# Optimization experiments

Measured on AMD Instinct MI355X. Metric: run time of the kernel, lower is better.

Reference implementation:

```python
import jax, jax.numpy as jnp
import numpy as np

V, H, B, S = 32000, 512, 64, 128


def _cell(x, h, c, wih, whh, bih, bhh):
    # PyTorch LSTMCell: gates = x@Wih^T + bih + h@Whh^T + bhh; order i,f,g,o
    g = x @ wih.T + bih + h @ whh.T + bhh
    i, f, gg, o = jnp.split(g, 4, axis=-1)
    c2 = jax.nn.sigmoid(f) * c + jax.nn.sigmoid(i) * jnp.tanh(gg)
    return jax.nn.sigmoid(o) * jnp.tanh(c2), c2


def setup_inputs() -> dict:
    key = jax.random.key(0)
    ks = jax.random.split(key, 30)
    def nrm(k, shape, s=0.05):
        return jax.random.normal(k, shape, jnp.float32) * s
    a1 = float(np.sqrt(6.0 / (B + H)))      # xavier bound for [B, H] state
    a2 = float(np.sqrt(6.0 / (B + 2 * H)))  # xavier bound for [B, 2H] state
    return {
        "x": jax.random.randint(ks[0], (B, S), 0, V),
        "emb": nrm(ks[1], (V, H)),
        "h0f": jax.random.uniform(ks[2], (B, H), jnp.float32, -a1, a1),
        "c0f": jax.random.uniform(ks[3], (B, H), jnp.float32, -a1, a1),
        "h0b": jax.random.uniform(ks[4], (B, H), jnp.float32, -a1, a1),
        "c0b": jax.random.uniform(ks[5], (B, H), jnp.float32, -a1, a1),
        "h01": jax.random.uniform(ks[6], (B, 2 * H), jnp.float32, -a2, a2),
        "h02": jax.random.uniform(ks[7], (B, 2 * H), jnp.float32, -a2, a2),
        "c02": jax.random.uniform(ks[8], (B, 2 * H), jnp.float32, -a2, a2),
        "wih_f": nrm(ks[9], (4 * H, H)), "whh_f": nrm(ks[10], (4 * H, H)),
        "bih_f": nrm(ks[11], (4 * H,)), "bhh_f": nrm(ks[12], (4 * H,)),
        "wih_b": nrm(ks[13], (4 * H, H)), "whh_b": nrm(ks[14], (4 * H, H)),
        "bih_b": nrm(ks[15], (4 * H,)), "bhh_b": nrm(ks[16], (4 * H,)),
        "wih1": nrm(ks[17], (8 * H, 2 * H)), "whh1": nrm(ks[18], (8 * H, 2 * H)),
        "bih1": nrm(ks[19], (8 * H,)), "bhh1": nrm(ks[20], (8 * H,)),
        "wih2": nrm(ks[21], (8 * H, 2 * H)), "whh2": nrm(ks[22], (8 * H, 2 * H)),
        "bih2": nrm(ks[23], (8 * H,)), "bhh2": nrm(ks[24], (8 * H,)),
        "wlin": nrm(ks[25], (V, 2 * H)), "blin": nrm(ks[26], (V,)),
    }


def reference(x, emb, h0f, c0f, h0b, c0b, h01, h02, c02,
              wih_f, whh_f, bih_f, bhh_f, wih_b, whh_b, bih_b, bhh_b,
              wih1, whh1, bih1, bhh1, wih2, whh2, bih2, bhh2, wlin, blin):
    E = emb.at[0].set(0.0)           # padding_idx=0
    out = E[x].reshape(S, B, H)      # faithful to torch .view(seq, batch, -1)

    def fstep(carry, xt):
        h, c = _cell(xt, carry[0], carry[1], wih_f, whh_f, bih_f, bhh_f)
        return (h, c), h
    _, fwd = jax.lax.scan(fstep, (h0f, c0f), out)

    def bstep(carry, xt):
        h, c = _cell(xt, carry[0], carry[1], wih_b, whh_b, bih_b, bhh_b)
        return (h, c), h
    _, bwd = jax.lax.scan(bstep, (h0b, c0b), out[::-1])  # appended in reversed order

    def sstep(carry, fb):
        h1, h2, c2 = carry
        xin = jnp.concatenate([fb[0], fb[1]], axis=1)
        # faithful to source: lstm_1 is fed cs_lstm_2 as its cell state; its own c is discarded
        h1n, _c1 = _cell(xin, h1, c2, wih1, whh1, bih1, bhh1)
        # dropout(p=0.2) is identity in eval / reference mode
        h2n, c2n = _cell(h1n, h2, c2, wih2, whh2, bih2, bhh2)
        return (h1n, h2n, c2n), None
    (h1, h2, c2), _ = jax.lax.scan(sstep, (h01, h02, c02), (fwd, bwd))

    return h2 @ wlin.T + blin  # [B, V]
```

## Files before the change

### kernel.cpp

```cpp
#include <hip/hip_runtime.h>
#include <stdint.h>
#include <stddef.h>

typedef uint16_t u16_t;
typedef uint32_t u32_t;
typedef short s16x8 __attribute__((ext_vector_type(8)));
typedef uint16_t u16x4v __attribute__((ext_vector_type(4)));
typedef uint16_t u16x8v __attribute__((ext_vector_type(8)));
typedef float f32x4 __attribute__((ext_vector_type(4)));

#define DEV static __device__ __forceinline__

DEV u16_t f2bf(float f) {
  u32_t u = __float_as_uint(f);
  u += 0x7fffu + ((u >> 16) & 1u);
  return (u16_t)(u >> 16);
}
DEV float sig_(float x) { return 1.f / (1.f + __expf(-x)); }
DEV float th_(float x) {
  x = fminf(15.f, fmaxf(-15.f, x));
  float e = __expf(2.f * x);
  return (e - 1.f) / (e + 1.f);
}


__global__ void k_buildWC(const float* __restrict__ wih, const float* __restrict__ whh,
                          const float* __restrict__ bih, const float* __restrict__ bhh,
                          u16_t* __restrict__ WC, float* __restrict__ bs, int HH)
{
  const int K = HH * 2;
  const int nk8 = K >> 3;
  const long total = (long)HH * 4 * nk8;
  long idx = (long)blockIdx.x * blockDim.x + threadIdx.x;
  if (idx >= total) return;
  int p = (int)(idx / nk8);
  int k = (int)(idx - (long)p * nk8) << 3;
  int q = (p >> 4) & 3;
  int orig = q * HH + ((p >> 6) << 4) + (p & 15);
  const float* s = (k < HH) ? (wih + (size_t)orig * HH + k)
                            : (whh + (size_t)orig * HH + (k - HH));
  f32x4 a = *(const f32x4*)s;
  f32x4 b = *(const f32x4*)(s + 4);
  u16x8v o;
  o[0]=f2bf(a[0]); o[1]=f2bf(a[1]); o[2]=f2bf(a[2]); o[3]=f2bf(a[3]);
  o[4]=f2bf(b[0]); o[5]=f2bf(b[1]); o[6]=f2bf(b[2]); o[7]=f2bf(b[3]);
  *(u16x8v*)(WC + (size_t)p * K + k) = o;
  if (k == 0) bs[p] = bih[orig] + bhh[orig];
}

__global__ void k_init(const float* __restrict__ h0f, const float* __restrict__ h0b,
                       const float* __restrict__ h01, const float* __restrict__ h02,
                       u16_t* __restrict__ XIN0, u16_t* __restrict__ H1i, u16_t* __restrict__ H2i)
{
  int i = blockIdx.x * 256 + threadIdx.x;
  if (i >= 64 * 1024) return;
  int b = i >> 10, d = i & 1023;
  XIN0[i] = f2bf(d < 512 ? h0f[b * 512 + d] : h0b[b * 512 + (d - 512)]);
  H1i[i] = f2bf(h01[i]);
  H2i[i] = f2bf(h02[i]);
}

__global__ void k_emb(const int* __restrict__ x, const float* __restrict__ emb,
                      u16_t* __restrict__ Xemb)
{
  int idx = blockIdx.x * 256 + threadIdx.x;
  if (idx >= 524288) return;
  int sb = idx >> 6;
  int h0 = (idx & 63) << 3;
  int token = x[(sb >> 7) * 128 + (sb & 127)];
  u16x8v o = {0,0,0,0,0,0,0,0};
  if (token != 0) {
    const float* e = emb + (size_t)token * 512 + h0;
    f32x4 a = *(const f32x4*)e;
    f32x4 b = *(const f32x4*)(e + 4);
    o[0]=f2bf(a[0]); o[1]=f2bf(a[1]); o[2]=f2bf(a[2]); o[3]=f2bf(a[3]);
    o[4]=f2bf(b[0]); o[5]=f2bf(b[1]); o[6]=f2bf(b[2]); o[7]=f2bf(b[3]);
  }
  *(u16x8v*)(Xemb + (size_t)sb * 512 + h0) = o;
}

template<int W>
DEV void stage_chunkT(u16_t* smem, const u16_t* src, int ld, int wave, int lane)
{
#pragma unroll
  for (int j = 0; j < 64 / W; ++j) {
    int r = j * W + wave;
    s16x8 v = *(const s16x8*)(src + (size_t)r * ld + lane * 8);
    *(s16x8*)((char*)smem + r * 1024 + ((lane * 16) ^ ((r & 7) << 4))) = v;
  }
}

DEV s16x8 ld_afrag(const u16_t* smem, int m, int s, int lane)
{
  int r = m * 16 + (lane & 15);
  int off = (s * 64 + ((lane >> 4) << 4)) ^ ((r & 7) << 4);
  return *(const s16x8*)((const char*)smem + r * 1024 + off);
}

DEV void chunk_stream(u16_t* smem, f32x4 acc[4], const u16_t* a, int ld,
                      const u16_t* wptr, int wave, int lane)
{
  __syncthreads();
  stage_chunkT<8>(smem, a, ld, wave, lane);
  __syncthreads();
#pragma unroll
  for (int s = 0; s < 16; ++s) {
    s16x8 bf = *(const s16x8*)(wptr + s * 32);
#pragma unroll
    for (int m = 0; m < 4; ++m) {
      s16x8 af = ld_afrag(smem, m, s, lane);
      acc[m] = __builtin_amdgcn_mfma_f32_16x16x32_bf16(af, bf, acc[m], 0, 0, 0);
    }
  }
}

DEV void chunk_reg(u16_t* smem, f32x4 acc[4], const u16_t* a, int ld,
                   const s16x8 wr[16], int wave, int lane)
{
  __syncthreads();
  stage_chunkT<8>(smem, a, ld, wave, lane);
  __syncthreads();
#pragma unroll
  for (int s = 0; s < 16; ++s) {
#pragma unroll
    for (int m = 0; m < 4; ++m) {
      s16x8 af = ld_afrag(smem, m, s, lane);
      acc[m] = __builtin_amdgcn_mfma_f32_16x16x32_bf16(af, wr[s], acc[m], 0, 0, 0);
    }
  }
}

DEV void acc_to_ex(float* ex, const f32x4 acc[4], int wave, int lane)
{
#pragma unroll
  for (int m = 0; m < 4; ++m)
#pragma unroll
    for (int r = 0; r < 4; ++r)
      ex[wave * 1024 + (m * 16 + ((lane >> 4) << 2) + r) * 16 + (lane & 15)] = acc[m][r];
}

DEV void ast8(void* p, const void* v)
{
  unsigned long long u; __builtin_memcpy(&u, v, 8);
  __hip_atomic_store((unsigned long long*)p, u, __ATOMIC_RELAXED, __HIP_MEMORY_SCOPE_AGENT);
}

DEV void wait_flags(u32_t* f, int n, int tid)
{
  if (tid < 64) {
    int guard = 0;
    for (;;) {
      u32_t v = (tid < n) ? __hip_atomic_load(f + tid, __ATOMIC_RELAXED, __HIP_MEMORY_SCOPE_AGENT) : 1u;
      if (__all(v != 0)) break;
      if (++guard > (1 << 22)) break;
      __builtin_amdgcn_s_sleep(1);
    }
  }
  __builtin_amdgcn_fence(__ATOMIC_ACQUIRE, "workgroup");
  __syncthreads();
}

DEV void set_flag(u32_t* f, int tid)
{
  __syncthreads();
  if (tid == 0) {
    __builtin_amdgcn_fence(__ATOMIC_RELEASE, "workgroup");
    __hip_atomic_store(f, 1u, __ATOMIC_RELAXED, __HIP_MEMORY_SCOPE_AGENT);
  }
}

struct RP {
  const u16_t *WCf, *WCb, *WC1, *WC2;
  const float *bsf, *bsb, *bs1, *bs2;
  const u16_t *Xemb;
  u16_t *XIN, *H1, *H2;
  float *C2;
  u32_t *FLC, *FLA, *FLB;
  const float *c0f, *c0b, *c02;
};

__global__ __launch_bounds__(512, 2) void k_rnn(RP P)
{
  __shared__ u16_t smem[32768];
  const int tid = threadIdx.x;
  const int wave = tid >> 6, lane = tid & 63;
  const int wg = blockIdx.x;
  const int b  = tid >> 3;
  const int d0 = (tid & 7) << 2;
  const int gl = d0 >> 4;
  const int jj = d0 & 15;
  const f32x4 vzero = {0.f, 0.f, 0.f, 0.f};

  if (wg < 32) {
    const bool cfwd = wg < 16;
    const int G = cfwd ? wg : wg - 16;
    const u16_t* WCc = cfwd ? P.WCf : P.WCb;
    const float* bsc = cfwd ? P.bsf : P.bsb;
    const float* c0 = cfwd ? P.c0f : P.c0b;
    float c_cell[4];
#pragma unroll
    for (int i = 0; i < 4; ++i) c_cell[i] = c0[b * 512 + G * 32 + d0 + i];
    const u16_t* wrow = WCc + (size_t)(G * 128 + wave * 16 + (lane & 15)) * 1024
                        + ((lane >> 4) << 3);
    s16x8 wL[16];
#pragma unroll
    for (int s = 0; s < 16; ++s) wL[s] = *(const s16x8*)(wrow + 512 + s * 32);

    for (int t = 0; t < 128; ++t) {
      f32x4 acc[4] = {vzero, vzero, vzero, vzero};
      int trow = cfwd ? t : 127 - t;
      chunk_stream(smem, acc, P.Xemb + (size_t)trow * 32768, 512, wrow, wave, lane);
      if (t > 0) wait_flags(P.FLC + (t - 1) * 32 + (cfwd ? 0 : 16), 16, tid);
      chunk_reg(smem, acc, P.XIN + (size_t)t * 65536 + (cfwd ? 0 : 512), 1024, wL, wave, lane);
      __syncthreads();
      float* ex = (float*)smem;
      acc_to_ex(ex, acc, wave, lane);
      __syncthreads();
      u16x4v hv;
#pragma unroll
      for (int i = 0; i < 4; ++i) {
        int j = jj + i;
        float gq[4];
#pragma unroll
        for (int q = 0; q < 4; ++q)
          gq[q] = ex[(gl * 4 + q) * 1024 + b * 16 + j] + bsc[G * 128 + gl * 64 + q * 16 + j];
        float c = sig_(gq[1]) * c_cell[i] + sig_(gq[0]) * th_(gq[2]);
        c_cell[i] = c;
        hv[i] = f2bf(sig_(gq[3]) * th_(c));
      }
      ast8(P.XIN + (size_t)(t + 1) * 65536 + b * 1024 + (cfwd ? 0 : 512) + G * 32 + d0, &hv);
      set_flag(P.FLC + t * 32 + wg, tid);
    }
  } else if (wg < 64) {
    const int G = wg - 32;
    const u16_t* wrow = P.WC1 + (size_t)(G * 128 + wave * 16 + (lane & 15)) * 2048
                        + ((lane >> 4) << 3);
    s16x8 wL[32];
#pragma unroll
    for (int s = 0; s < 32; ++s) wL[s] = *(const s16x8*)(wrow + 1024 + s * 32);

    for (int u = 0; u < 128; ++u) {
      f32x4 acc[4] = {vzero, vzero, vzero, vzero};
      const u16_t* xin = P.XIN + (size_t)(u + 1) * 65536;
      wait_flags(P.FLC + u * 32, 16, tid);
      chunk_stream(smem, acc, xin, 1024, wrow, wave, lane);
      wait_flags(P.FLC + u * 32 + 16, 16, tid);
      chunk_stream(smem, acc, xin + 512, 1024, wrow + 512, wave, lane);
      if (u > 0) wait_flags(P.FLB + (u - 1) * 32 + G, 1, tid);
      const u16_t* h1p = P.H1 + (size_t)u * 65536;
      chunk_reg(smem, acc, h1p, 1024, wL, wave, lane);
      chunk_reg(smem, acc, h1p + 512, 1024, wL + 16, wave, lane);
      __syncthreads();
      float* ex = (float*)smem;
      acc_to_ex(ex, acc, wave, lane);
      __syncthreads();
      const float* c2p = (u == 0) ? (P.c02 + b * 1024 + G * 32 + d0)
                                  : (P.C2 + (size_t)u * 65536 + b * 1024 + G * 32 + d0);
      u16x4v hv;
#pragma unroll
      for (int i = 0; i < 4; ++i) {
        int j = jj + i;
        float gq[4];
#pragma unroll
        for (int q = 0; q < 4; ++q)
          gq[q] = ex[(gl * 4 + q) * 1024 + b * 16 + j] + P.bs1[G * 128 + gl * 64 + q * 16 + j];
        float c1 = sig_(gq[1]) * c2p[i] + sig_(gq[0]) * th_(gq[2]);
        hv[i] = f2bf(sig_(gq[3]) * th_(c1));
      }
      ast8(P.H1 + (size_t)(u + 1) * 65536 + b * 1024 + G * 32 + d0, &hv);
      set_flag(P.FLA + u * 32 + G, tid);
    }
  } else {
    const int G = wg - 64;
    const u16_t* wrow = P.WC2 + (size_t)(G * 128 + wave * 16 + (lane & 15)) * 2048
                        + ((lane >> 4) << 3);
    s16x8 wL[32];
#pragma unroll
    for (int s = 0; s < 32; ++s) wL[s] = *(const s16x8*)(wrow + s * 32);
    float c2r[4];
#pragma unroll
    for (int i = 0; i < 4; ++i) c2r[i] = P.c02[b * 1024 + G * 32 + d0 + i];

    for (int u = 0; u < 128; ++u) {
      f32x4 acc[4] = {vzero, vzero, vzero, vzero};
      const u16_t* h2p = P.H2 + (size_t)u * 65536;
      if (u > 0) wait_flags(P.FLB + (u - 1) * 32, 16, tid);
      chunk_stream(smem, acc, h2p, 1024, wrow + 1024, wave, lane);
      if (u > 0) wait_flags(P.FLB + (u - 1) * 32 + 16, 16, tid);
      chunk_stream(smem, acc, h2p + 512, 1024, wrow + 1536, wave, lane);
      const u16_t* h1n = P.H1 + (size_t)(u + 1) * 65536;
      wait_flags(P.FLA + u * 32, 16, tid);
      chunk_reg(smem, acc, h1n, 1024, wL, wave, lane);
      wait_flags(P.FLA + u * 32 + 16, 16, tid);
      chunk_reg(smem, acc, h1n + 512, 1024, wL + 16, wave, lane);
      __syncthreads();
      float* ex = (float*)smem;
      acc_to_ex(ex, acc, wave, lane);
      __syncthreads();
      u16x4v hv; float c2o[4];
#pragma unroll
      for (int i = 0; i < 4; ++i) {
        int j = jj + i;
        float gq[4];
#pragma unroll
        for (int q = 0; q < 4; ++q)
          gq[q] = ex[(gl * 4 + q) * 1024 + b * 16 + j] + P.bs2[G * 128 + gl * 64 + q * 16 + j];
        float c2n = sig_(gq[1]) * c2r[i] + sig_(gq[0]) * th_(gq[2]);
        c2r[i] = c2n; c2o[i] = c2n;
        hv[i] = f2bf(sig_(gq[3]) * th_(c2n));
      }
      ast8(P.H2 + (size_t)(u + 1) * 65536 + b * 1024 + G * 32 + d0, &hv);
      float* c2dst = P.C2 + (size_t)(u + 1) * 65536 + b * 1024 + G * 32 + d0;
      ast8(c2dst, &c2o[0]);
      ast8(c2dst + 2, &c2o[2]);
      set_flag(P.FLB + u * 32 + G, tid);
    }
  }
}

__global__ __launch_bounds__(256, 1) void k_logits(const u16_t* __restrict__ h2,
                                                   const float* __restrict__ wlin,
                                                   const float* __restrict__ blin,
                                                   float* __restrict__ out)
{
  __shared__ u16_t smem[32768];
  const int tid = threadIdx.x, wave = tid >> 6, lane = tid & 63;
  const int n0 = blockIdx.x * 128 + wave * 32;
  const f32x4 vzero = {0.f, 0.f, 0.f, 0.f};
  f32x4 acc[2][4];
#pragma unroll
  for (int nt = 0; nt < 2; ++nt)
#pragma unroll
    for (int m = 0; m < 4; ++m) acc[nt][m] = vzero;

  for (int c = 0; c < 2; ++c) {
    __syncthreads();
    stage_chunkT<4>(smem, h2 + c * 512, 1024, wave, lane);
    __syncthreads();
#pragma unroll
    for (int s = 0; s < 16; ++s) {
#pragma unroll
      for (int nt = 0; nt < 2; ++nt) {
        const float* wp = wlin + (size_t)(n0 + nt * 16 + (lane & 15)) * 1024
                          + c * 512 + s * 32 + ((lane >> 4) << 3);
        f32x4 w0 = *(const f32x4*)wp;
        f32x4 w1 = *(const f32x4*)(wp + 4);
        s16x8 bf;
        bf[0]=(short)f2bf(w0[0]); bf[1]=(short)f2bf(w0[1]);
        bf[2]=(short)f2bf(w0[2]); bf[3]=(short)f2bf(w0[3]);
        bf[4]=(short)f2bf(w1[0]); bf[5]=(short)f2bf(w1[1]);
        bf[6]=(short)f2bf(w1[2]); bf[7]=(short)f2bf(w1[3]);
#pragma unroll
        for (int m = 0; m < 4; ++m) {
          s16x8 af = ld_afrag(smem, m, s, lane);
          acc[nt][m] = __builtin_amdgcn_mfma_f32_16x16x32_bf16(af, bf, acc[nt][m], 0, 0, 0);
        }
      }
    }
  }
#pragma unroll
  for (int nt = 0; nt < 2; ++nt) {
    int col = n0 + nt * 16 + (lane & 15);
    float bl = blin[col];
#pragma unroll
    for (int m = 0; m < 4; ++m)
#pragma unroll
      for (int r = 0; r < 4; ++r) {
        int row = m * 16 + ((lane >> 4) << 2) + r;
        out[(size_t)row * 32000 + col] = acc[nt][m][r] + bl;
      }
  }
}

extern "C" void kernel_launch(void* const* d_in, const int* in_sizes, int n_in,
                              void* d_out, int out_size, void* d_ws, size_t ws_size,
                              hipStream_t stream)
{
  (void)in_sizes; (void)n_in; (void)out_size;
  const int*   x     = (const int*)d_in[0];
  const float* emb   = (const float*)d_in[1];
  const float* h0f   = (const float*)d_in[2];
  const float* c0f   = (const float*)d_in[3];
  const float* h0b   = (const float*)d_in[4];
  const float* c0b   = (const float*)d_in[5];
  const float* h01   = (const float*)d_in[6];
  const float* h02   = (const float*)d_in[7];
  const float* c02   = (const float*)d_in[8];
  const float* wih_f = (const float*)d_in[9];
  const float* whh_f = (const float*)d_in[10];
  const float* bih_f = (const float*)d_in[11];
  const float* bhh_f = (const float*)d_in[12];
  const float* wih_b = (const float*)d_in[13];
  const float* whh_b = (const float*)d_in[14];
  const float* bih_b = (const float*)d_in[15];
  const float* bhh_b = (const float*)d_in[16];
  const float* wih1  = (const float*)d_in[17];
  const float* whh1  = (const float*)d_in[18];
  const float* bih1  = (const float*)d_in[19];
  const float* bhh1  = (const float*)d_in[20];
  const float* wih2  = (const float*)d_in[21];
  const float* whh2  = (const float*)d_in[22];
  const float* bih2  = (const float*)d_in[23];
  const float* bhh2  = (const float*)d_in[24];
  const float* wlin  = (const float*)d_in[25];
  const float* blin  = (const float*)d_in[26];

  char* ws = (char*)d_ws;
  size_t off = 0;
  auto take = [&](size_t n) { char* p = ws + off; off += (n + 255) & ~(size_t)255; return p; };

  u16_t* WCf  = (u16_t*)take(2048UL * 1024 * 2);
  u16_t* WCb  = (u16_t*)take(2048UL * 1024 * 2);
  u16_t* WC1  = (u16_t*)take(4096UL * 2048 * 2);
  u16_t* WC2  = (u16_t*)take(4096UL * 2048 * 2);
  float* bsf  = (float*)take(2048UL * 4);
  float* bsb  = (float*)take(2048UL * 4);
  float* bs1  = (float*)take(4096UL * 4);
  float* bs2  = (float*)take(4096UL * 4);
  u16_t* Xemb = (u16_t*)take(8192UL * 512 * 2);
  u16_t* XIN  = (u16_t*)take(129UL * 65536 * 2);
  u16_t* H1   = (u16_t*)take(129UL * 65536 * 2);
  u16_t* H2   = (u16_t*)take(129UL * 65536 * 2);
  float* C2   = (float*)take(129UL * 65536 * 4);
  char* flagbase = ws + off;
  u32_t* FLC  = (u32_t*)take(128UL * 32 * 4);
  u32_t* FLA  = (u32_t*)take(128UL * 32 * 4);
  u32_t* FLB  = (u32_t*)take(128UL * 32 * 4);
  size_t flagbytes = (size_t)((ws + off) - flagbase);

  if (off > ws_size) return;

  hipMemsetAsync(flagbase, 0, flagbytes, stream);

  k_buildWC<<<1024, 256, 0, stream>>>(wih_f, whh_f, bih_f, bhh_f, WCf, bsf, 512);
  k_buildWC<<<1024, 256, 0, stream>>>(wih_b, whh_b, bih_b, bhh_b, WCb, bsb, 512);
  k_buildWC<<<4096, 256, 0, stream>>>(wih1, whh1, bih1, bhh1, WC1, bs1, 1024);
  k_buildWC<<<4096, 256, 0, stream>>>(wih2, whh2, bih2, bhh2, WC2, bs2, 1024);
  k_init<<<256, 256, 0, stream>>>(h0f, h0b, h01, h02, XIN, H1, H2);
  k_emb<<<2048, 256, 0, stream>>>(x, emb, Xemb);

  RP P;
  P.WCf = WCf; P.WCb = WCb; P.WC1 = WC1; P.WC2 = WC2;
  P.bsf = bsf; P.bsb = bsb; P.bs1 = bs1; P.bs2 = bs2;
  P.Xemb = Xemb; P.XIN = XIN; P.H1 = H1; P.H2 = H2; P.C2 = C2;
  P.FLC = FLC; P.FLA = FLA; P.FLB = FLB;
  P.c0f = c0f; P.c0b = c0b; P.c02 = c02;
  k_rnn<<<96, 512, 0, stream>>>(P);

  k_logits<<<250, 256, 0, stream>>>(H2 + 128UL * 65536, wlin, blin, (float*)d_out);
}
```

Before: 2.463 ms.

## Load recurrent A-fragments directly from global and move cell-state wait later

```diff
diff --git a/kernel.cpp b/kernel.cpp
--- a/kernel.cpp
+++ b/kernel.cpp
@@ -114,17 +114,14 @@
   }
 }
 
-DEV void chunk_reg(u16_t* smem, f32x4 acc[4], const u16_t* a, int ld,
-                   const s16x8 wr[16], int wave, int lane)
-{
-  __syncthreads();
-  stage_chunkT<8>(smem, a, ld, wave, lane);
-  __syncthreads();
+DEV void dchunk(f32x4 acc[4], const u16_t* a, int ld, const s16x8 wr[16], int lane)
+{
 #pragma unroll
   for (int s = 0; s < 16; ++s) {
 #pragma unroll
     for (int m = 0; m < 4; ++m) {
-      s16x8 af = ld_afrag(smem, m, s, lane);
+      s16x8 af = *(const s16x8*)(a + (size_t)(m * 16 + (lane & 15)) * ld
+                                 + s * 32 + ((lane >> 4) << 3));
       acc[m] = __builtin_amdgcn_mfma_f32_16x16x32_bf16(af, wr[s], acc[m], 0, 0, 0);
     }
   }
@@ -168,6 +165,11 @@
     __hip_atomic_store(f, 1u, __ATOMIC_RELAXED, __HIP_MEMORY_SCOPE_AGENT);
   }
 }
+
+#define PIN16(W) { _Pragma("unroll") for (int _s = 0; _s < 16; ++_s) \
+                     asm volatile("" : "+v"((W)[_s])); }
+#define PIN32(W) { _Pragma("unroll") for (int _s = 0; _s < 32; ++_s) \
+                     asm volatile("" : "+v"((W)[_s])); }
 
 struct RP {
   const u16_t *WCf, *WCb, *WC1, *WC2;
@@ -205,13 +207,14 @@
     s16x8 wL[16];
 #pragma unroll
     for (int s = 0; s < 16; ++s) wL[s] = *(const s16x8*)(wrow + 512 + s * 32);
+    PIN16(wL);
 
     for (int t = 0; t < 128; ++t) {
       f32x4 acc[4] = {vzero, vzero, vzero, vzero};
       int trow = cfwd ? t : 127 - t;
       chunk_stream(smem, acc, P.Xemb + (size_t)trow * 32768, 512, wrow, wave, lane);
       if (t > 0) wait_flags(P.FLC + (t - 1) * 32 + (cfwd ? 0 : 16), 16, tid);
-      chunk_reg(smem, acc, P.XIN + (size_t)t * 65536 + (cfwd ? 0 : 512), 1024, wL, wave, lane);
+      dchunk(acc, P.XIN + (size_t)t * 65536 + (cfwd ? 0 : 512), 1024, wL, lane);
       __syncthreads();
       float* ex = (float*)smem;
       acc_to_ex(ex, acc, wave, lane);
@@ -238,22 +241,24 @@
     s16x8 wL[32];
 #pragma unroll
     for (int s = 0; s < 32; ++s) wL[s] = *(const s16x8*)(wrow + 1024 + s * 32);
+    PIN32(wL);
 
     for (int u = 0; u < 128; ++u) {
       f32x4 acc[4] = {vzero, vzero, vzero, vzero};
+      wait_flags(P.FLC + u * 32, 32, tid);
       const u16_t* xin = P.XIN + (size_t)(u + 1) * 65536;
-      wait_flags(P.FLC + u * 32, 16, tid);
       chunk_stream(smem, acc, xin, 1024, wrow, wave, lane);
-      wait_flags(P.FLC + u * 32 + 16, 16, tid);
       chunk_stream(smem, acc, xin + 512, 1024, wrow + 512, wave, lane);
-      if (u > 0) wait_flags(P.FLB + (u - 1) * 32 + G, 1, tid);
       const u16_t* h1p = P.H1 + (size_t)u * 65536;
-      chunk_reg(smem, acc, h1p, 1024, wL, wave, lane);
-      chunk_reg(smem, acc, h1p + 512, 1024, wL + 16, wave, lane);
+      if (u > 0) wait_flags(P.FLA + (u - 1) * 32, 16, tid);
+      dchunk(acc, h1p, 1024, wL, lane);
+      if (u > 0) wait_flags(P.FLA + (u - 1) * 32, 32, tid);
+      dchunk(acc, h1p + 512, 1024, wL + 16, lane);
       __syncthreads();
       float* ex = (float*)smem;
       acc_to_ex(ex, acc, wave, lane);
       __syncthreads();
+      if (u > 0) wait_flags(P.FLB + (u - 1) * 32 + G, 1, tid);
       const float* c2p = (u == 0) ? (P.c02 + b * 1024 + G * 32 + d0)
                                   : (P.C2 + (size_t)u * 65536 + b * 1024 + G * 32 + d0);
       u16x4v hv;
@@ -277,6 +282,7 @@
     s16x8 wL[32];
 #pragma unroll
     for (int s = 0; s < 32; ++s) wL[s] = *(const s16x8*)(wrow + s * 32);
+    PIN32(wL);
     float c2r[4];
 #pragma unroll
     for (int i = 0; i < 4; ++i) c2r[i] = P.c02[b * 1024 + G * 32 + d0 + i];
@@ -286,13 +292,13 @@
       const u16_t* h2p = P.H2 + (size_t)u * 65536;
       if (u > 0) wait_flags(P.FLB + (u - 1) * 32, 16, tid);
       chunk_stream(smem, acc, h2p, 1024, wrow + 1024, wave, lane);
-      if (u > 0) wait_flags(P.FLB + (u - 1) * 32 + 16, 16, tid);
+      if (u > 0) wait_flags(P.FLB + (u - 1) * 32, 32, tid);
       chunk_stream(smem, acc, h2p + 512, 1024, wrow + 1536, wave, lane);
       const u16_t* h1n = P.H1 + (size_t)(u + 1) * 65536;
       wait_flags(P.FLA + u * 32, 16, tid);
-      chunk_reg(smem, acc, h1n, 1024, wL, wave, lane);
-      wait_flags(P.FLA + u * 32 + 16, 16, tid);
-      chunk_reg(smem, acc, h1n + 512, 1024, wL + 16, wave, lane);
+      dchunk(acc, h1n, 1024, wL, lane);
+      wait_flags(P.FLA + u * 32, 32, tid);
+      dchunk(acc, h1n + 512, 1024, wL + 16, lane);
       __syncthreads();
       float* ex = (float*)smem;
       acc_to_ex(ex, acc, wave, lane);
```

New measurement: 5.773 ms. 134% more time.
